# Performance work log

Measured on AMD Instinct MI355X. Metric: run time of the kernel, lower is better.

## Reference

```python
import jax, jax.numpy as jnp
import numpy as np

N, IN_DIM, OUT_DIM = 16384, 256, 128

def setup_inputs() -> dict:
    key = jax.random.key(0)
    ks = jax.random.split(key, 7)
    s_in = 1.0 / np.sqrt(IN_DIM)
    return {
        "x": jax.random.normal(ks[0], (N, IN_DIM), dtype=jnp.float32),
        "Wq": jax.random.uniform(ks[1], (IN_DIM, OUT_DIM), jnp.float32, -s_in, s_in),
        "bq": jax.random.uniform(ks[2], (OUT_DIM,), jnp.float32, -s_in, s_in),
        "Wk": jax.random.uniform(ks[3], (IN_DIM, OUT_DIM), jnp.float32, -s_in, s_in),
        "bk": jax.random.uniform(ks[4], (OUT_DIM,), jnp.float32, -s_in, s_in),
        "Wv": jax.random.uniform(ks[5], (IN_DIM, OUT_DIM), jnp.float32, -s_in, s_in),
        "bv": jax.random.uniform(ks[6], (OUT_DIM,), jnp.float32, -s_in, s_in),
    }

def reference(x, Wq, bq, Wk, bk, Wv, bv):
    # QKV projections: [N, out_dim]
    q = x @ Wq + bq
    k = x @ Wk + bk
    v = x @ Wv + bv
    # Unscaled dot-product affinity [N, N], row softmax, weighted sum of V.
    affinity = jax.nn.softmax(q @ k.T, axis=-1)
    return affinity @ v
```

## Files before the change

### kernel.cpp

```cpp
#include <hip/hip_runtime.h>

typedef _Float16 f16;
typedef _Float16 f16x2 __attribute__((ext_vector_type(2)));
typedef _Float16 f16x8 __attribute__((ext_vector_type(8)));
typedef float f32x4 __attribute__((ext_vector_type(4)));
typedef float f32x16 __attribute__((ext_vector_type(16)));

#define MFMA16(a, b, c) __builtin_amdgcn_mfma_f32_16x16x32_f16((a), (b), (c), 0, 0, 0)
#define MFMA32(a, b, c) __builtin_amdgcn_mfma_f32_32x32x16_f16((a), (b), (c), 0, 0, 0)
#define LOG2E 1.44269504088896340736f
#define SHIFT_L2 28.8539008178f

#define NROWS 16384
#define INDIM 256
#define ODIM 128
#define NQT 128

__global__ __launch_bounds__(256) void prep_kernel(
    const float* __restrict__ Wq, const float* __restrict__ Wk, const float* __restrict__ Wv,
    f16* __restrict__ WqT, f16* __restrict__ WkT, f16* __restrict__ WvT) {
    int w = blockIdx.x >> 5;
    int local = blockIdx.x & 31;
    const float* W = (w == 0) ? Wq : ((w == 1) ? Wk : Wv);
    f16* WT = (w == 0) ? WqT : ((w == 1) ? WkT : WvT);
    int j0 = local * 1024 + threadIdx.x;
#pragma unroll
    for (int t = 0; t < 4; t++) {
        int j = j0 + t * 256;
        int n = j >> 8;
        int k = j & 255;
        WT[j] = (f16)W[k * ODIM + n];
    }
}

__global__ __launch_bounds__(256) void proj_kernel(
    const float* __restrict__ x,
    const f16* __restrict__ WqT, const f16* __restrict__ WkT, const f16* __restrict__ WvT,
    const float* __restrict__ bq, const float* __restrict__ bk, const float* __restrict__ bv,
    f16* __restrict__ Qh, f16* __restrict__ Kh, f16* __restrict__ Vt) {
    int blk = blockIdx.x;
    int wave = threadIdx.x >> 6;
    int lane = threadIdx.x & 63;
    int l16 = lane & 15, quad = lane >> 4;

    __shared__ __align__(16) f16 Vs[128 * 72];

    if (blk < 256) {
        int r0 = blk * 64 + wave * 16;
        f16x8 ax[8];
        const float* xp = x + (size_t)(r0 + l16) * INDIM + quad * 8;
#pragma unroll
        for (int kc = 0; kc < 8; kc++) {
            f32x4 u = *(const f32x4*)(xp + kc * 32);
            f32x4 v = *(const f32x4*)(xp + kc * 32 + 4);
            f16x8 t;
            t[0] = (f16)u[0]; t[1] = (f16)u[1]; t[2] = (f16)u[2]; t[3] = (f16)u[3];
            t[4] = (f16)v[0]; t[5] = (f16)v[1]; t[6] = (f16)v[2]; t[7] = (f16)v[3];
            ax[kc] = t;
        }
#pragma unroll
        for (int nt = 0; nt < 8; nt++) {
            f32x4 aq = {0.f, 0.f, 0.f, 0.f}, ak = {0.f, 0.f, 0.f, 0.f};
            const f16* wq = WqT + (nt * 16 + l16) * INDIM + quad * 8;
            const f16* wk = WkT + (nt * 16 + l16) * INDIM + quad * 8;
#pragma unroll
            for (int kc = 0; kc < 8; kc++) {
                f16x8 bqf = *(const f16x8*)(wq + kc * 32);
                f16x8 bkf = *(const f16x8*)(wk + kc * 32);
                aq = MFMA16(ax[kc], bqf, aq);
                ak = MFMA16(ax[kc], bkf, ak);
            }
            int col = nt * 16 + l16;
            float biasq = bq[col], biask = bk[col];
#pragma unroll
            for (int r = 0; r < 4; r++) {
                int row = r0 + quad * 4 + r;
                Qh[(size_t)row * ODIM + col] = (f16)(aq[r] + biasq);
                Kh[(size_t)row * ODIM + col] = (f16)(ak[r] + biask);
            }
        }
    } else {
        int i0 = (blk - 256) * 64;
        int iw = wave * 16;
        f16x8 bx[8];
        const float* xp = x + (size_t)(i0 + iw + l16) * INDIM + quad * 8;
#pragma unroll
        for (int kc = 0; kc < 8; kc++) {
            f32x4 u = *(const f32x4*)(xp + kc * 32);
            f32x4 v = *(const f32x4*)(xp + kc * 32 + 4);
            f16x8 t;
            t[0] = (f16)u[0]; t[1] = (f16)u[1]; t[2] = (f16)u[2]; t[3] = (f16)u[3];
            t[4] = (f16)v[0]; t[5] = (f16)v[1]; t[6] = (f16)v[2]; t[7] = (f16)v[3];
            bx[kc] = t;
        }
#pragma unroll
        for (int dt = 0; dt < 8; dt++) {
            f32x4 acc = {0.f, 0.f, 0.f, 0.f};
            const f16* wv = WvT + (dt * 16 + l16) * INDIM + quad * 8;
#pragma unroll
            for (int kc = 0; kc < 8; kc++) {
                f16x8 a = *(const f16x8*)(wv + kc * 32);
                acc = MFMA16(a, bx[kc], acc);
            }
#pragma unroll
            for (int r = 0; r < 4; r++) {
                int d = dt * 16 + quad * 4 + r;
                Vs[d * 72 + iw + l16] = (f16)(acc[r] + bv[d]);
            }
        }
        __syncthreads();
        int d = threadIdx.x >> 1, c = (threadIdx.x & 1) * 32;
        const f16* srcp = Vs + d * 72 + c;
        f16* dstp = Vt + (size_t)d * NROWS + i0 + c;
#pragma unroll
        for (int i2 = 0; i2 < 4; i2++)
            *(f16x8*)(dstp + i2 * 8) = *(const f16x8*)(srcp + i2 * 8);
    }
}

__global__ __launch_bounds__(256, 2) void flash_kernel(
    const f16* __restrict__ Qh, const f16* __restrict__ Kh, const f16* __restrict__ Vt,
    float* __restrict__ Opart, float* __restrict__ lbuf, float* __restrict__ Out,
    int nsplit, int niter) {
    int blk = blockIdx.x;
    int qt = blk & (NQT - 1);
    int sp = blk >> 7;
    int tid = threadIdx.x;
    int wave = tid >> 6;
    int lane = tid & 63;
    int l32 = lane & 31;
    int h = lane >> 5;

    __shared__ __align__(16) f16 Kl[64 * 136];
    __shared__ __align__(16) f16 Vl[128 * 72];

    int rowbase = qt * 128 + wave * 32;

    f16x8 qf[8];
    {
        const f16* qp = Qh + (size_t)(rowbase + l32) * ODIM + h * 8;
#pragma unroll
        for (int ks = 0; ks < 8; ks++) qf[ks] = *(const f16x8*)(qp + ks * 16);
    }

    f32x16 o[4];
#pragma unroll
    for (int dt = 0; dt < 4; dt++)
#pragma unroll
        for (int g = 0; g < 16; g++) o[dt][g] = 0.f;
    float l_r = 0.f;

    int kr_row = tid >> 2, kr_c = (tid & 3) * 32;
    int vr_d = tid >> 1, vr_h = (tid & 1) * 32;

    int j0 = sp * (niter * 64);

    f16x8 kr[4], vr[4];
    {
        const f16* kp = Kh + (size_t)(j0 + kr_row) * ODIM + kr_c;
        const f16* vp = Vt + (size_t)vr_d * NROWS + j0 + vr_h;
#pragma unroll
        for (int i = 0; i < 4; i++) {
            kr[i] = *(const f16x8*)(kp + i * 8);
            vr[i] = *(const f16x8*)(vp + i * 8);
        }
    }

    for (int it = 0; it < niter; ++it) {
        __syncthreads();
        {
            f16* kd = Kl + kr_row * 136 + kr_c;
            f16* vd = Vl + vr_d * 72 + vr_h;
#pragma unroll
            for (int i = 0; i < 4; i++) {
                *(f16x8*)(kd + i * 8) = kr[i];
                *(f16x8*)(vd + i * 8) = vr[i];
            }
        }
        __syncthreads();
        if (it + 1 < niter) {
            int jn = j0 + 64;
            const f16* kp = Kh + (size_t)(jn + kr_row) * ODIM + kr_c;
            const f16* vp = Vt + (size_t)vr_d * NROWS + jn + vr_h;
#pragma unroll
            for (int i = 0; i < 4; i++) {
                kr[i] = *(const f16x8*)(kp + i * 8);
                vr[i] = *(const f16x8*)(vp + i * 8);
            }
        }
        f32x16 st[2];
#pragma unroll
        for (int ct = 0; ct < 2; ct++) {
#pragma unroll
            for (int g = 0; g < 16; g++) st[ct][g] = 0.f;
        }
#pragma unroll
        for (int ct = 0; ct < 2; ct++) {
            const f16* kp = Kl + (ct * 32 + l32) * 136 + h * 8;
#pragma unroll
            for (int ks = 0; ks < 8; ks++) {
                f16x8 kf = *(const f16x8*)(kp + ks * 16);
                st[ct] = MFMA32(kf, qf[ks], st[ct]);
            }
        }
        int pk[2][8];
#pragma unroll
        for (int ct = 0; ct < 2; ct++) {
#pragma unroll
            for (int w = 0; w < 8; w++) {
                float a = __builtin_amdgcn_exp2f(fmaf(st[ct][2 * w], LOG2E, -SHIFT_L2));
                float b = __builtin_amdgcn_exp2f(fmaf(st[ct][2 * w + 1], LOG2E, -SHIFT_L2));
                l_r += a + b;
                pk[ct][w] = __builtin_bit_cast(int, __builtin_amdgcn_cvt_pkrtz(a, b));
            }
        }
        f16x8 pf[4];
#pragma unroll
        for (int ks = 0; ks < 4; ks++) {
            int ct = ks >> 1, b = (ks & 1) * 4;
            int off0 = h ? pk[ct][b] : pk[ct][b + 2];
            int off1 = h ? pk[ct][b + 1] : pk[ct][b + 3];
            int R0 = __shfl_xor(off0, 32, 64);
            int R1 = __shfl_xor(off1, 32, 64);
            union { int i[4]; f16x8 v; } u;
            u.i[0] = h ? R0 : pk[ct][b];
            u.i[1] = h ? R1 : pk[ct][b + 1];
            u.i[2] = h ? pk[ct][b + 2] : R0;
            u.i[3] = h ? pk[ct][b + 3] : R1;
            pf[ks] = u.v;
        }
#pragma unroll
        for (int dt = 0; dt < 4; dt++) {
            const f16* vp = Vl + (dt * 32 + l32) * 72 + h * 8;
#pragma unroll
            for (int ks = 0; ks < 4; ks++) {
                f16x8 vf = *(const f16x8*)(vp + ks * 16);
                o[dt] = MFMA32(vf, pf[ks], o[dt]);
            }
        }
        j0 += 64;
    }

    l_r += __shfl_xor(l_r, 32, 64);

    if (nsplit == 1) {
        float inv = 1.f / l_r;
        float* op = Out + (size_t)(rowbase + l32) * ODIM;
#pragma unroll
        for (int dt = 0; dt < 4; dt++)
#pragma unroll
            for (int gg = 0; gg < 4; gg++) {
                f32x4 v = {o[dt][4 * gg] * inv, o[dt][4 * gg + 1] * inv,
                           o[dt][4 * gg + 2] * inv, o[dt][4 * gg + 3] * inv};
                *(f32x4*)(op + dt * 32 + 8 * gg + 4 * h) = v;
            }
    } else {
        float* op = Opart + ((size_t)sp * NROWS + rowbase + l32) * ODIM;
#pragma unroll
        for (int dt = 0; dt < 4; dt++)
#pragma unroll
            for (int gg = 0; gg < 4; gg++) {
                f32x4 v = {o[dt][4 * gg], o[dt][4 * gg + 1],
                           o[dt][4 * gg + 2], o[dt][4 * gg + 3]};
                *(f32x4*)(op + dt * 32 + 8 * gg + 4 * h) = v;
            }
        if (lane < 32)
            lbuf[(size_t)sp * NROWS + rowbase + l32] = l_r;
    }
}

__global__ __launch_bounds__(256) void merge_kernel(const float* __restrict__ Opart,
                                                    const float* __restrict__ lbuf,
                                                    float* __restrict__ out, int nsplit) {
    int idx = blockIdx.x * 256 + threadIdx.x;
    int row = idx >> 7;
    float acc = 0.f, den = 0.f;
    for (int s = 0; s < nsplit; s++) {
        acc += Opart[(size_t)s * (NROWS * ODIM) + idx];
        den += lbuf[(size_t)s * NROWS + row];
    }
    out[idx] = acc / den;
}

extern "C" void kernel_launch(void* const* d_in, const int* in_sizes, int n_in,
                              void* d_out, int out_size, void* d_ws, size_t ws_size,
                              hipStream_t stream) {
    const float* x  = (const float*)d_in[0];
    const float* Wq = (const float*)d_in[1];
    const float* bq = (const float*)d_in[2];
    const float* Wk = (const float*)d_in[3];
    const float* bk = (const float*)d_in[4];
    const float* Wv = (const float*)d_in[5];
    const float* bv = (const float*)d_in[6];
    float* out = (float*)d_out;
    char* ws = (char*)d_ws;

    const size_t WT_BYTES = (size_t)ODIM * INDIM * sizeof(f16);
    const size_t QKV_BYTES = (size_t)NROWS * ODIM * sizeof(f16);
    f16* WqT = (f16*)(ws);
    f16* WkT = (f16*)(ws + WT_BYTES);
    f16* WvT = (f16*)(ws + 2 * WT_BYTES);
    f16* Qh  = (f16*)(ws + 3 * WT_BYTES);
    f16* Kh  = (f16*)(ws + 3 * WT_BYTES + QKV_BYTES);
    f16* Vt  = (f16*)(ws + 3 * WT_BYTES + 2 * QKV_BYTES);
    size_t base = 3 * WT_BYTES + 3 * QKV_BYTES;

    const size_t OPART_BYTES = (size_t)NROWS * ODIM * sizeof(float);
    const size_t L_BYTES = (size_t)NROWS * sizeof(float);

    int nsplit = 1;
    if (ws_size >= base + 4 * (OPART_BYTES + L_BYTES)) nsplit = 4;
    else if (ws_size >= base + 2 * (OPART_BYTES + L_BYTES)) nsplit = 2;

    float* Opart = (float*)(ws + base);
    float* lbuf  = (float*)(ws + base + (size_t)nsplit * OPART_BYTES);

    prep_kernel<<<96, 256, 0, stream>>>(Wq, Wk, Wv, WqT, WkT, WvT);
    proj_kernel<<<512, 256, 0, stream>>>(x, WqT, WkT, WvT, bq, bk, bv, Qh, Kh, Vt);
    flash_kernel<<<NQT * nsplit, 256, 0, stream>>>(Qh, Kh, Vt, Opart, lbuf, out, nsplit,
                                                   (NROWS / 64) / nsplit);
    if (nsplit > 1)
        merge_kernel<<<(NROWS * ODIM) / 256, 256, 0, stream>>>(Opart, lbuf, out, nsplit);
}
```

Baseline: 259.9 us.

## Double query rows per wave to reuse K/V tiles, vectorize merge

Each wave now processes two 32-row query tiles (256 rows per block, half as many blocks), so every K and V fragment loaded from LDS feeds two MFMAs. This halves LDS and global K/V traffic per query row, at the cost of roughly double the accumulator registers, so occupancy drops to one block per SIMD set. The V projection now writes transposed values straight to global memory without the LDS staging pass, which makes those stores strided. The merge kernel reads and writes four floats per thread.

```diff
diff --git a/kernel.cpp b/kernel.cpp
--- a/kernel.cpp
+++ b/kernel.cpp
@@ -1,7 +1,6 @@
 #include <hip/hip_runtime.h>
 
 typedef _Float16 f16;
-typedef _Float16 f16x2 __attribute__((ext_vector_type(2)));
 typedef _Float16 f16x8 __attribute__((ext_vector_type(8)));
 typedef float f32x4 __attribute__((ext_vector_type(4)));
 typedef float f32x16 __attribute__((ext_vector_type(16)));
@@ -14,7 +13,7 @@
 #define NROWS 16384
 #define INDIM 256
 #define ODIM 128
-#define NQT 128
+#define NQT 64
 
 __global__ __launch_bounds__(256) void prep_kernel(
     const float* __restrict__ Wq, const float* __restrict__ Wk, const float* __restrict__ Wv,
@@ -43,8 +42,6 @@
     int lane = threadIdx.x & 63;
     int l16 = lane & 15, quad = lane >> 4;
 
-    __shared__ __align__(16) f16 Vs[128 * 72];
-
     if (blk < 256) {
         int r0 = blk * 64 + wave * 16;
         f16x8 ax[8];
@@ -80,10 +77,9 @@
             }
         }
     } else {
-        int i0 = (blk - 256) * 64;
-        int iw = wave * 16;
+        int i0 = (blk - 256) * 64 + wave * 16;
         f16x8 bx[8];
-        const float* xp = x + (size_t)(i0 + iw + l16) * INDIM + quad * 8;
+        const float* xp = x + (size_t)(i0 + l16) * INDIM + quad * 8;
 #pragma unroll
         for (int kc = 0; kc < 8; kc++) {
             f32x4 u = *(const f32x4*)(xp + kc * 32);
@@ -105,26 +101,19 @@
 #pragma unroll
             for (int r = 0; r < 4; r++) {
                 int d = dt * 16 + quad * 4 + r;
-                Vs[d * 72 + iw + l16] = (f16)(acc[r] + bv[d]);
-            }
-        }
-        __syncthreads();
-        int d = threadIdx.x >> 1, c = (threadIdx.x & 1) * 32;
-        const f16* srcp = Vs + d * 72 + c;
-        f16* dstp = Vt + (size_t)d * NROWS + i0 + c;
-#pragma unroll
-        for (int i2 = 0; i2 < 4; i2++)
-            *(f16x8*)(dstp + i2 * 8) = *(const f16x8*)(srcp + i2 * 8);
-    }
-}
-
-__global__ __launch_bounds__(256, 2) void flash_kernel(
+                Vt[(size_t)d * NROWS + i0 + l16] = (f16)(acc[r] + bv[d]);
+            }
+        }
+    }
+}
+
+__global__ __launch_bounds__(256, 1) void flash_kernel(
     const f16* __restrict__ Qh, const f16* __restrict__ Kh, const f16* __restrict__ Vt,
     float* __restrict__ Opart, float* __restrict__ lbuf, float* __restrict__ Out,
     int nsplit, int niter) {
     int blk = blockIdx.x;
     int qt = blk & (NQT - 1);
-    int sp = blk >> 7;
+    int sp = blk >> 6;
     int tid = threadIdx.x;
     int wave = tid >> 6;
     int lane = tid & 63;
@@ -134,21 +123,24 @@
     __shared__ __align__(16) f16 Kl[64 * 136];
     __shared__ __align__(16) f16 Vl[128 * 72];
 
-    int rowbase = qt * 128 + wave * 32;
-
-    f16x8 qf[8];
-    {
-        const f16* qp = Qh + (size_t)(rowbase + l32) * ODIM + h * 8;
-#pragma unroll
-        for (int ks = 0; ks < 8; ks++) qf[ks] = *(const f16x8*)(qp + ks * 16);
-    }
-
-    f32x16 o[4];
-#pragma unroll
-    for (int dt = 0; dt < 4; dt++)
-#pragma unroll
-        for (int g = 0; g < 16; g++) o[dt][g] = 0.f;
-    float l_r = 0.f;
+    int rowbase = qt * 256 + wave * 64;
+
+    f16x8 qf[2][8];
+#pragma unroll
+    for (int t = 0; t < 2; t++) {
+        const f16* qp = Qh + (size_t)(rowbase + t * 32 + l32) * ODIM + h * 8;
+#pragma unroll
+        for (int ks = 0; ks < 8; ks++) qf[t][ks] = *(const f16x8*)(qp + ks * 16);
+    }
+
+    f32x16 o[2][4];
+#pragma unroll
+    for (int t = 0; t < 2; t++)
+#pragma unroll
+        for (int dt = 0; dt < 4; dt++)
+#pragma unroll
+            for (int g = 0; g < 16; g++) o[t][dt][g] = 0.f;
+    float l_r[2] = {0.f, 0.f};
 
     int kr_row = tid >> 2, kr_c = (tid & 3) * 32;
     int vr_d = tid >> 1, vr_h = (tid & 1) * 32;
@@ -188,98 +180,111 @@
                 vr[i] = *(const f16x8*)(vp + i * 8);
             }
         }
-        f32x16 st[2];
+        int pk[2][2][8];
 #pragma unroll
         for (int ct = 0; ct < 2; ct++) {
-#pragma unroll
-            for (int g = 0; g < 16; g++) st[ct][g] = 0.f;
-        }
-#pragma unroll
-        for (int ct = 0; ct < 2; ct++) {
+            f32x16 st0, st1;
+#pragma unroll
+            for (int g = 0; g < 16; g++) { st0[g] = 0.f; st1[g] = 0.f; }
             const f16* kp = Kl + (ct * 32 + l32) * 136 + h * 8;
 #pragma unroll
             for (int ks = 0; ks < 8; ks++) {
                 f16x8 kf = *(const f16x8*)(kp + ks * 16);
-                st[ct] = MFMA32(kf, qf[ks], st[ct]);
-            }
-        }
-        int pk[2][8];
-#pragma unroll
-        for (int ct = 0; ct < 2; ct++) {
+                st0 = MFMA32(kf, qf[0][ks], st0);
+                st1 = MFMA32(kf, qf[1][ks], st1);
+            }
 #pragma unroll
             for (int w = 0; w < 8; w++) {
-                float a = __builtin_amdgcn_exp2f(fmaf(st[ct][2 * w], LOG2E, -SHIFT_L2));
-                float b = __builtin_amdgcn_exp2f(fmaf(st[ct][2 * w + 1], LOG2E, -SHIFT_L2));
-                l_r += a + b;
-                pk[ct][w] = __builtin_bit_cast(int, __builtin_amdgcn_cvt_pkrtz(a, b));
-            }
-        }
-        f16x8 pf[4];
-#pragma unroll
-        for (int ks = 0; ks < 4; ks++) {
-            int ct = ks >> 1, b = (ks & 1) * 4;
-            int off0 = h ? pk[ct][b] : pk[ct][b + 2];
-            int off1 = h ? pk[ct][b + 1] : pk[ct][b + 3];
-            int R0 = __shfl_xor(off0, 32, 64);
-            int R1 = __shfl_xor(off1, 32, 64);
-            union { int i[4]; f16x8 v; } u;
-            u.i[0] = h ? R0 : pk[ct][b];
-            u.i[1] = h ? R1 : pk[ct][b + 1];
-            u.i[2] = h ? pk[ct][b + 2] : R0;
-            u.i[3] = h ? pk[ct][b + 3] : R1;
-            pf[ks] = u.v;
-        }
+                float a0 = __builtin_amdgcn_exp2f(fmaf(st0[2 * w], LOG2E, -SHIFT_L2));
+                float b0 = __builtin_amdgcn_exp2f(fmaf(st0[2 * w + 1], LOG2E, -SHIFT_L2));
+                l_r[0] += a0 + b0;
+                pk[ct][0][w] = __builtin_bit_cast(int, __builtin_amdgcn_cvt_pkrtz(a0, b0));
+                float a1 = __builtin_amdgcn_exp2f(fmaf(st1[2 * w], LOG2E, -SHIFT_L2));
+                float b1 = __builtin_amdgcn_exp2f(fmaf(st1[2 * w + 1], LOG2E, -SHIFT_L2));
+                l_r[1] += a1 + b1;
+                pk[ct][1][w] = __builtin_bit_cast(int, __builtin_amdgcn_cvt_pkrtz(a1, b1));
+            }
+        }
+        f16x8 pf[2][4];
+#pragma unroll
+        for (int t = 0; t < 2; t++)
+#pragma unroll
+            for (int ks = 0; ks < 4; ks++) {
+                int ct = ks >> 1, b = (ks & 1) * 4;
+                int off0 = h ? pk[ct][t][b] : pk[ct][t][b + 2];
+                int off1 = h ? pk[ct][t][b + 1] : pk[ct][t][b + 3];
+                int R0 = __shfl_xor(off0, 32, 64);
+                int R1 = __shfl_xor(off1, 32, 64);
+                union { int i[4]; f16x8 v; } u;
+                u.i[0] = h ? R0 : pk[ct][t][b];
+                u.i[1] = h ? R1 : pk[ct][t][b + 1];
+                u.i[2] = h ? pk[ct][t][b + 2] : R0;
+                u.i[3] = h ? pk[ct][t][b + 3] : R1;
+                pf[t][ks] = u.v;
+            }
 #pragma unroll
         for (int dt = 0; dt < 4; dt++) {
             const f16* vp = Vl + (dt * 32 + l32) * 72 + h * 8;
 #pragma unroll
             for (int ks = 0; ks < 4; ks++) {
                 f16x8 vf = *(const f16x8*)(vp + ks * 16);
-                o[dt] = MFMA32(vf, pf[ks], o[dt]);
+                o[0][dt] = MFMA32(vf, pf[0][ks], o[0][dt]);
+                o[1][dt] = MFMA32(vf, pf[1][ks], o[1][dt]);
             }
         }
         j0 += 64;
     }
 
-    l_r += __shfl_xor(l_r, 32, 64);
+#pragma unroll
+    for (int t = 0; t < 2; t++) l_r[t] += __shfl_xor(l_r[t], 32, 64);
 
     if (nsplit == 1) {
-        float inv = 1.f / l_r;
-        float* op = Out + (size_t)(rowbase + l32) * ODIM;
-#pragma unroll
-        for (int dt = 0; dt < 4; dt++)
-#pragma unroll
-            for (int gg = 0; gg < 4; gg++) {
-                f32x4 v = {o[dt][4 * gg] * inv, o[dt][4 * gg + 1] * inv,
-                           o[dt][4 * gg + 2] * inv, o[dt][4 * gg + 3] * inv};
-                *(f32x4*)(op + dt * 32 + 8 * gg + 4 * h) = v;
-            }
+#pragma unroll
+        for (int t = 0; t < 2; t++) {
+            float inv = 1.f / l_r[t];
+            float* op = Out + (size_t)(rowbase + t * 32 + l32) * ODIM;
+#pragma unroll
+            for (int dt = 0; dt < 4; dt++)
+#pragma unroll
+                for (int gg = 0; gg < 4; gg++) {
+                    f32x4 v = {o[t][dt][4 * gg] * inv, o[t][dt][4 * gg + 1] * inv,
+                               o[t][dt][4 * gg + 2] * inv, o[t][dt][4 * gg + 3] * inv};
+                    *(f32x4*)(op + dt * 32 + 8 * gg + 4 * h) = v;
+                }
+        }
     } else {
-        float* op = Opart + ((size_t)sp * NROWS + rowbase + l32) * ODIM;
-#pragma unroll
-        for (int dt = 0; dt < 4; dt++)
-#pragma unroll
-            for (int gg = 0; gg < 4; gg++) {
-                f32x4 v = {o[dt][4 * gg], o[dt][4 * gg + 1],
-                           o[dt][4 * gg + 2], o[dt][4 * gg + 3]};
-                *(f32x4*)(op + dt * 32 + 8 * gg + 4 * h) = v;
-            }
-        if (lane < 32)
-            lbuf[(size_t)sp * NROWS + rowbase + l32] = l_r;
+#pragma unroll
+        for (int t = 0; t < 2; t++) {
+            float* op = Opart + ((size_t)sp * NROWS + rowbase + t * 32 + l32) * ODIM;
+#pragma unroll
+            for (int dt = 0; dt < 4; dt++)
+#pragma unroll
+                for (int gg = 0; gg < 4; gg++) {
+                    f32x4 v = {o[t][dt][4 * gg], o[t][dt][4 * gg + 1],
+                               o[t][dt][4 * gg + 2], o[t][dt][4 * gg + 3]};
+                    *(f32x4*)(op + dt * 32 + 8 * gg + 4 * h) = v;
+                }
+            if (lane < 32)
+                lbuf[(size_t)sp * NROWS + rowbase + t * 32 + l32] = l_r[t];
+        }
     }
 }
 
 __global__ __launch_bounds__(256) void merge_kernel(const float* __restrict__ Opart,
                                                     const float* __restrict__ lbuf,
                                                     float* __restrict__ out, int nsplit) {
-    int idx = blockIdx.x * 256 + threadIdx.x;
+    int idx = (blockIdx.x * 256 + threadIdx.x) * 4;
     int row = idx >> 7;
-    float acc = 0.f, den = 0.f;
+    f32x4 acc = {0.f, 0.f, 0.f, 0.f};
+    float den = 0.f;
     for (int s = 0; s < nsplit; s++) {
-        acc += Opart[(size_t)s * (NROWS * ODIM) + idx];
+        f32x4 v = *(const f32x4*)(Opart + (size_t)s * (NROWS * ODIM) + idx);
+        acc[0] += v[0]; acc[1] += v[1]; acc[2] += v[2]; acc[3] += v[3];
         den += lbuf[(size_t)s * NROWS + row];
     }
-    out[idx] = acc / den;
+    float inv = 1.f / den;
+    f32x4 r = {acc[0] * inv, acc[1] * inv, acc[2] * inv, acc[3] * inv};
+    *(f32x4*)(out + idx) = r;
 }
 
 extern "C" void kernel_launch(void* const* d_in, const int* in_sizes, int n_in,
@@ -320,5 +325,5 @@
     flash_kernel<<<NQT * nsplit, 256, 0, stream>>>(Qh, Kh, Vt, Opart, lbuf, out, nsplit,
                                                    (NROWS / 64) / nsplit);
     if (nsplit > 1)
-        merge_kernel<<<(NROWS * ODIM) / 256, 256, 0, stream>>>(Opart, lbuf, out, nsplit);
-}
+        merge_kernel<<<(NROWS * ODIM) / 1024, 256, 0, stream>>>(Opart, lbuf, out, nsplit);
+}
```

Result: slower. 282.5 us (+8.7%).
